# Optimization experiments

Measured on AMD Instinct MI355X. Metric: run time of the kernel, lower is better.

The kernel has to match this reference:

```python
import jax, jax.numpy as jnp
import numpy as np

# ---- problem sizes / hyperparameters (init_kwargs) ----
B, N = 1024, 512          # batch, variable dim
M_INEQ, M_EQ = 512, 16    # inequality / equality constraint counts
ALPHA = 0.05              # PGD step size
MAX_ITER = 3              # PGD iterations (self.max_iter)
RHO = 1.0                 # ADMM penalty for the projection QP
ADMM_ITERS = 15           # inner QP-solver iterations (replaces QPFunction interior point)


def setup_inputs() -> dict:
    key = jax.random.key(0)
    k1, k2, k3, k4 = jax.random.split(key, 4)
    c = jax.random.normal(k1, (B, N), jnp.float32)
    G = jax.random.normal(k2, (M_INEQ, N), jnp.float32) / np.float32(np.sqrt(N))
    A = jax.random.normal(k3, (M_EQ, N), jnp.float32) / np.float32(np.sqrt(N))
    z0 = jax.random.normal(k4, (N,), jnp.float32)  # known feasible point
    b = A @ z0
    h = G @ z0 + jnp.float32(0.5)  # strict feasibility margin
    return {"c": c, "G": G, "h": h, "A": A, "b": b}


def _project(x, G, h, A, b):
    """Batched Euclidean projection: argmin_z ||z - x||^2 s.t. Gz<=h, Az=b.
    Mathematically identical to QPFunction(2*I, -2*x, G, h, A, b); solved with
    a fixed-iteration ADMM sharing one precomputed KKT factor across the batch.
    """
    n = x.shape[-1]
    me = A.shape[0]
    bs = x.shape[0]
    # KKT matrix for the equality-constrained z-update: [[I + rho G^T G, A^T],[A, 0]]
    K = jnp.block([
        [jnp.eye(n, dtype=x.dtype) + RHO * (G.T @ G), A.T],
        [A, jnp.zeros((me, me), x.dtype)],
    ])
    Kinv = jnp.linalg.inv(K)  # (n+me, n+me), shared across batch & iterations
    b_rhs = jnp.broadcast_to(b, (bs, me))

    def z_from(s, u):
        # rhs = [x + rho * G^T (h - s - u); b], batched over B
        rhs = jnp.concatenate([x + RHO * ((h - s - u) @ G), b_rhs], axis=-1)
        return (rhs @ Kinv.T)[:, :n]  # [B, N]

    s = jnp.maximum(0.0, h - x @ G.T)  # slack init at z0 = x
    u = jnp.zeros_like(s)              # scaled dual

    def step(carry, _):
        s, u = carry
        z = z_from(s, u)
        Gz = z @ G.T                             # [B, M_INEQ]
        s2 = jnp.maximum(0.0, h - Gz - u)        # s-update (projection onto s>=0)
        u2 = u + Gz + s2 - h                     # dual update
        return (s2, u2), None

    (s, u), _ = jax.lax.scan(step, (s, u), None, length=ADMM_ITERS)
    return z_from(s, u)


def reference(c, G, h, A, b):
    # x = cvx_blank(c): initial feasible iterate (projection of c onto the polytope)
    x = _project(c, G, h, A, b)
    for _ in range(MAX_ITER):  # PGD loop (small fixed count)
        grad = x - c                # grad_f(x_i, c_i) for f = 0.5||x - c||^2 (batched)
        x = x - ALPHA * grad        # gradient step
        x = _project(x, G, h, A, b) # QP projection step (QPFunction equivalent)
    return x
```

## Files before the change

kernel.cpp:

```cpp
#include <hip/hip_runtime.h>
#include <hip/hip_bf16.h>

#define BB 1024
#define NN 512
#define MI 512
#define ME 16
#define ALPHA 0.05f
#define NS_ITERS 8
#define ADMM_IT 15

typedef __attribute__((ext_vector_type(8))) short short8;
typedef __attribute__((ext_vector_type(4))) float float4v;

__device__ inline short f2bf(float v) {
    __hip_bfloat16 b = __float2bfloat16(v);
    return *reinterpret_cast<short*>(&b);
}
__device__ inline float bf2f(short s) {
    __hip_bfloat16 b = *reinterpret_cast<__hip_bfloat16*>(&s);
    return __bfloat162float(b);
}
__device__ inline void split_store(float v, short* __restrict__ hi, short* __restrict__ lo, size_t idx) {
    short h = f2bf(v);
    hi[idx] = h;
    lo[idx] = f2bf(v - bf2f(h));
}

__global__ void detect_dtype_k(const unsigned short* __restrict__ g_raw,
                               float* __restrict__ flag) {
    __shared__ int cnt;
    int tid = threadIdx.x;
    if (tid == 0) cnt = 0;
    __syncthreads();
    int local = 0;
    for (int i = tid; i < 8192; i += 256) {
        int e = (g_raw[i] >> 7) & 0xFF;
        if (e >= 0x83) local++;
    }
    atomicAdd(&cnt, local);
    __syncthreads();
    if (tid == 0) flag[0] = (cnt < 64) ? 1.0f : 0.0f;
}

__global__ void ingest_all_k(const void* __restrict__ c_raw, const void* __restrict__ G_raw,
                             const void* __restrict__ h_raw, const void* __restrict__ A_raw,
                             const void* __restrict__ b_raw,
                             float* __restrict__ cF, short* __restrict__ xh, short* __restrict__ xl,
                             float* __restrict__ GF, short* __restrict__ GFh, short* __restrict__ GFl,
                             float* __restrict__ hF, float* __restrict__ AF, float* __restrict__ bF,
                             const float* __restrict__ flag) {
    int i = blockIdx.x * 256 + threadIdx.x;
    bool isbf = flag[0] > 0.5f;
    #define RD(p, idx) (isbf ? __bfloat162float(((const __hip_bfloat16*)(p))[idx]) : ((const float*)(p))[idx])
    if (i < BB * NN) { float v = RD(c_raw, i); cF[i] = v; split_store(v, xh, xl, i); }
    if (i < MI * NN) { float v = RD(G_raw, i); GF[i] = v; split_store(v, GFh, GFl, i); }
    if (i < MI)      hF[i] = RD(h_raw, i);
    if (i < ME * NN) AF[i] = RD(A_raw, i);
    if (i < ME)      bF[i] = RD(b_raw, i);
    #undef RD
}

__global__ void transpose_split_k(const float* __restrict__ src,
                                  short* __restrict__ dh, short* __restrict__ dl) {
    __shared__ float t[32][33];
    int bx = blockIdx.x * 32, by = blockIdx.y * 32;
    int tx = threadIdx.x & 31, ty0 = threadIdx.x >> 5;
    for (int i = ty0; i < 32; i += 8) t[i][tx] = src[(by + i) * 512 + bx + tx];
    __syncthreads();
    for (int i = ty0; i < 32; i += 8)
        split_store(t[tx][i], dh, dl, (size_t)(bx + i) * 512 + by + tx);
}

__global__ void row_abs_sum_k(const float* __restrict__ Mm, float* __restrict__ rs) {
    int row = blockIdx.x, lane = threadIdx.x;
    float s = 0.f;
    for (int j = lane; j < NN; j += 64) s += fabsf(Mm[row * NN + j]);
    for (int off = 32; off; off >>= 1) s += __shfl_down(s, off);
    if (lane == 0) rs[row] = s;
}

__global__ void max_c0_k(const float* __restrict__ rs, float* __restrict__ c0s) {
    int lane = threadIdx.x;
    float m = 0.f;
    for (int i = lane; i < NN; i += 64) m = fmaxf(m, rs[i]);
    for (int off = 32; off; off >>= 1) m = fmaxf(m, __shfl_down(m, off));
    if (lane == 0) c0s[0] = 2.0f / (1.0f + m);
}

__global__ void init_X_k(float* __restrict__ X, short* __restrict__ Xhi,
                         short* __restrict__ Xlo, const float* __restrict__ c0s) {
    int idx = blockIdx.x * 256 + threadIdx.x;
    if (idx < NN * NN) {
        int i = idx / NN, j = idx - i * NN;
        float v = (i == j) ? c0s[0] : 0.f;
        X[idx] = v;
        split_store(v, Xhi, Xlo, idx);
    }
}

__global__ void inv16_k(const float* __restrict__ S, float* __restrict__ Si) {
    int r = threadIdx.x;
    float a[16], bI[16];
    #pragma unroll
    for (int j = 0; j < 16; ++j) {
        a[j]  = (r < 16) ? S[r * 16 + j] : 0.f;
        bI[j] = (r < 16 && j == r) ? 1.f : 0.f;
    }
    for (int k = 0; k < 16; ++k) {
        float pa[16], pb[16];
        #pragma unroll
        for (int j = 0; j < 16; ++j) { pa[j] = __shfl(a[j], k); pb[j] = __shfl(bI[j], k); }
        float inv = 1.0f / pa[k];
        if (r == k) {
            #pragma unroll
            for (int j = 0; j < 16; ++j) { a[j] = pa[j] * inv; bI[j] = pb[j] * inv; }
        } else {
            float f = a[k] * inv;
            #pragma unroll
            for (int j = 0; j < 16; ++j) {
                a[j]  = fmaf(-f, pa[j], a[j]);
                bI[j] = fmaf(-f, pb[j], bI[j]);
            }
        }
    }
    if (r < 16)
        #pragma unroll
        for (int j = 0; j < 16; ++j) Si[r * 16 + j] = bI[j];
}

__global__ void Y_k(const float* __restrict__ Minv, const float* __restrict__ AF,
                    float* __restrict__ Y) {
    int m = blockIdx.x;
    int wv = threadIdx.x >> 6, lane = threadIdx.x & 63;
    float mv[8];
    #pragma unroll
    for (int i = 0; i < 8; ++i) mv[i] = Minv[m * 512 + lane + i * 64];
    #pragma unroll
    for (int jj = 0; jj < 4; ++jj) {
        int j = wv * 4 + jj;
        float s = 0.f;
        #pragma unroll
        for (int i = 0; i < 8; ++i) s += mv[i] * AF[j * 512 + lane + i * 64];
        for (int off = 32; off; off >>= 1) s += __shfl_down(s, off);
        if (lane == 0) Y[m * 16 + j] = s;
    }
}

__global__ void Sm_k(const float* __restrict__ AF, const float* __restrict__ Y,
                     float* __restrict__ Sm) {
    int i = threadIdx.x >> 4, j = threadIdx.x & 15;
    float s = 0.f;
    #pragma unroll 8
    for (int k = 0; k < 512; ++k) s += AF[i * 512 + k] * Y[k * 16 + j];
    Sm[i * 16 + j] = s;
}

__global__ void T1zb_k(const float* __restrict__ Y, const float* __restrict__ Si,
                       const float* __restrict__ bF, float* __restrict__ T1,
                       float* __restrict__ zb) {
    int m = blockIdx.x * 16 + (threadIdx.x >> 4), j = threadIdx.x & 15;
    float s = 0.f;
    #pragma unroll
    for (int k = 0; k < 16; ++k) s += Y[m * 16 + k] * Si[k * 16 + j];
    T1[m * 16 + j] = s;
    float v = s * bF[j];
    v += __shfl_down(v, 8); v += __shfl_down(v, 4);
    v += __shfl_down(v, 2); v += __shfl_down(v, 1);
    if (j == 0) zb[m] = v;
}

__global__ void W1_k(const float* __restrict__ Minv, const float* __restrict__ T1,
                     const float* __restrict__ Y,
                     short* __restrict__ W1h, short* __restrict__ W1l) {
    int idx = blockIdx.x * 256 + threadIdx.x;
    int m = idx >> 9, n = idx & 511;
    float s = Minv[idx];
    #pragma unroll
    for (int k = 0; k < 16; ++k) s -= T1[m * 16 + k] * Y[n * 16 + k];
    split_store(s, W1h, W1l, idx);
}

__global__ void g0_k(const float* __restrict__ GF, const float* __restrict__ zb,
                     float* __restrict__ g0) {
    int m = blockIdx.x * 4 + (threadIdx.x >> 6);
    int lane = threadIdx.x & 63;
    float s = 0.f;
    #pragma unroll
    for (int i = 0; i < 8; ++i) s += GF[m * 512 + lane + i * 64] * zb[lane + i * 64];
    for (int off = 32; off; off >>= 1) s += __shfl_down(s, off);
    if (lane == 0) g0[m] = s;
}

#define CH 128
#define LDC 136

__global__ __launch_bounds__(256) void mfma_gemm2(
    const short* __restrict__ Ahi, const short* __restrict__ Alo,
    const short* __restrict__ Bhi, const short* __restrict__ Blo,
    float* __restrict__ C, short* __restrict__ Chi, short* __restrict__ Clo,
    const float* __restrict__ E, const float* __restrict__ v1,
    float* __restrict__ U, float* __restrict__ Xtra,
    const float* __restrict__ dtf, void* __restrict__ Out, int epi)
{
    __shared__ short Ash[2][16 * LDC];
    __shared__ short Bsh[2][64 * LDC];
    const int tid = threadIdx.x;
    const int wv = tid >> 6, ln = tid & 63;
    const int quad = ln >> 4, lr = ln & 15;
    const int m0 = blockIdx.y * 16, n0 = blockIdx.x * 64;

    float4v acc1 = {0.f, 0.f, 0.f, 0.f};
    float4v acc2 = {0.f, 0.f, 0.f, 0.f};

    short8 pa[2], pb[8];
    #pragma unroll
    for (int i = 0; i < 2; ++i) {
        int s = tid + 256 * i; int pl = s >> 8, rem = s & 255, row = rem >> 4, oct = rem & 15;
        const short* P = pl ? Alo : Ahi;
        pa[i] = *(const short8*)(P + (size_t)(m0 + row) * 512 + oct * 8);
    }
    #pragma unroll
    for (int i = 0; i < 8; ++i) {
        int s = tid + 256 * i; int pl = s >> 10, rem = s & 1023, row = rem >> 4, oct = rem & 15;
        const short* P = pl ? Blo : Bhi;
        pb[i] = *(const short8*)(P + (size_t)(n0 + row) * 512 + oct * 8);
    }

    for (int c = 0; c < 4; ++c) {
        if (c) __syncthreads();
        #pragma unroll
        for (int i = 0; i < 2; ++i) {
            int s = tid + 256 * i; int pl = s >> 8, rem = s & 255, row = rem >> 4, oct = rem & 15;
            *(short8*)&Ash[pl][row * LDC + oct * 8] = pa[i];
        }
        #pragma unroll
        for (int i = 0; i < 8; ++i) {
            int s = tid + 256 * i; int pl = s >> 10, rem = s & 1023, row = rem >> 4, oct = rem & 15;
            *(short8*)&Bsh[pl][row * LDC + oct * 8] = pb[i];
        }
        __syncthreads();
        if (c + 1 < 4) {
            int kb = (c + 1) * CH;
            #pragma unroll
            for (int i = 0; i < 2; ++i) {
                int s = tid + 256 * i; int pl = s >> 8, rem = s & 255, row = rem >> 4, oct = rem & 15;
                const short* P = pl ? Alo : Ahi;
                pa[i] = *(const short8*)(P + (size_t)(m0 + row) * 512 + kb + oct * 8);
            }
            #pragma unroll
            for (int i = 0; i < 8; ++i) {
                int s = tid + 256 * i; int pl = s >> 10, rem = s & 1023, row = rem >> 4, oct = rem & 15;
                const short* P = pl ? Blo : Bhi;
                pb[i] = *(const short8*)(P + (size_t)(n0 + row) * 512 + kb + oct * 8);
            }
        }
        #pragma unroll
        for (int ks = 0; ks < 4; ++ks) {
            int ko = (ks * 4 + quad) * 8;
            short8 ah = *(const short8*)&Ash[0][lr * LDC + ko];
            short8 al = *(const short8*)&Ash[1][lr * LDC + ko];
            short8 bh = *(const short8*)&Bsh[0][(wv * 16 + lr) * LDC + ko];
            short8 bl = *(const short8*)&Bsh[1][(wv * 16 + lr) * LDC + ko];
            acc1 = __builtin_amdgcn_mfma_f32_16x16x32_bf16(ah, bh, acc1, 0, 0, 0);
            acc2 = __builtin_amdgcn_mfma_f32_16x16x32_bf16(ah, bl, acc2, 0, 0, 0);
            acc2 = __builtin_amdgcn_mfma_f32_16x16x32_bf16(al, bh, acc2, 0, 0, 0);
        }
    }

    #pragma unroll
    for (int r = 0; r < 4; ++r) {
        int m = m0 + quad * 4 + r;
        int n = n0 + wv * 16 + lr;
        float a = acc1[r] + acc2[r];
        if (epi == 7) {
            int seg = n0 >> 9;
            int nl = n - (seg << 9);
            size_t idx = (size_t)m * 512 + nl;
            if (seg == 0) {
                float t0 = fminf(v1[nl], a);
                U[idx] = 0.f;
                Chi[idx] = f2bf(t0);
            } else if (seg == 1) {
                C[idx] = a + E[nl];
            } else {
                Xtra[idx] = a;
            }
            continue;
        }
        size_t idx = (size_t)m * 512 + n;
        if (epi == 0) {
            C[idx] = a;
            if (Chi) split_store(a, Chi, Clo, idx);
        } else if (epi == 1) {
            a += (m == n) ? 1.f : 0.f;
            C[idx] = a;
            split_store(a, Chi, Clo, idx);
        } else if (epi == 2) {
            a = 2.f * E[idx] - a;
            C[idx] = a;
            split_store(a, Chi, Clo, idx);
        } else if (epi == 6) {
            float z = a + E[idx] + v1[n];
            float xp = (1.0f - ALPHA) * z + ALPHA * Xtra[idx];
            split_store(xp, Chi, Clo, idx);
        } else if (epi == 8) {
            float z = a + E[idx] + v1[n];
            if (dtf[0] > 0.5f) ((__hip_bfloat16*)Out)[idx] = __float2bfloat16(z);
            else               ((float*)Out)[idx] = z;
        } else {
            split_store(a, Chi, Clo, idx);
        }
    }
}

__global__ __launch_bounds__(256) void admm_bf16_k(
    const short* __restrict__ Ab, const short* __restrict__ Bb,
    const float* __restrict__ q0, const float* __restrict__ hF,
    float* __restrict__ uB, short* __restrict__ dh, short* __restrict__ dl)
{
    __shared__ short As[16 * LDC];
    __shared__ short Bs[64 * LDC];
    const int tid = threadIdx.x;
    const int wv = tid >> 6, ln = tid & 63;
    const int quad = ln >> 4, lr = ln & 15;
    const int m0 = blockIdx.y * 16, n0 = blockIdx.x * 64;

    float4v acc1 = {0.f, 0.f, 0.f, 0.f};
    float4v acc2 = {0.f, 0.f, 0.f, 0.f};

    short8 pa, pb[4];
    {
        int row = tid >> 4, oct = tid & 15;
        pa = *(const short8*)(Ab + (size_t)(m0 + row) * 512 + oct * 8);
    }
    #pragma unroll
    for (int i = 0; i < 4; ++i) {
        int s = tid + 256 * i; int row = s >> 4, oct = s & 15;
        pb[i] = *(const short8*)(Bb + (size_t)(n0 + row) * 512 + oct * 8);
    }

    for (int c = 0; c < 4; ++c) {
        if (c) __syncthreads();
        {
            int row = tid >> 4, oct = tid & 15;
            *(short8*)&As[row * LDC + oct * 8] = pa;
        }
        #pragma unroll
        for (int i = 0; i < 4; ++i) {
            int s = tid + 256 * i; int row = s >> 4, oct = s & 15;
            *(short8*)&Bs[row * LDC + oct * 8] = pb[i];
        }
        __syncthreads();
        if (c + 1 < 4) {
            int kb = (c + 1) * CH;
            {
                int row = tid >> 4, oct = tid & 15;
                pa = *(const short8*)(Ab + (size_t)(m0 + row) * 512 + kb + oct * 8);
            }
            #pragma unroll
            for (int i = 0; i < 4; ++i) {
                int s = tid + 256 * i; int row = s >> 4, oct = s & 15;
                pb[i] = *(const short8*)(Bb + (size_t)(n0 + row) * 512 + kb + oct * 8);
            }
        }
        #pragma unroll
        for (int ks = 0; ks < 4; ++ks) {
            int ko = (ks * 4 + quad) * 8;
            short8 a = *(const short8*)&As[lr * LDC + ko];
            short8 b = *(const short8*)&Bs[(wv * 16 + lr) * LDC + ko];
            if (ks & 1) acc2 = __builtin_amdgcn_mfma_f32_16x16x32_bf16(a, b, acc2, 0, 0, 0);
            else        acc1 = __builtin_amdgcn_mfma_f32_16x16x32_bf16(a, b, acc1, 0, 0, 0);
        }
    }

    #pragma unroll
    for (int r = 0; r < 4; ++r) {
        int m = m0 + quad * 4 + r;
        int n = n0 + wv * 16 + lr;
        size_t idx = (size_t)m * 512 + n;
        float gz = acc1[r] + acc2[r] + q0[idx];
        float hn = hF[n];
        float w = hn - gz - uB[idx];
        uB[idx] = fmaxf(0.f, -w);
        float t2 = hn - fabsf(w);
        short hh = f2bf(t2);
        dh[idx] = hh;
        if (dl) dl[idx] = f2bf(t2 - bf2f(hh));
    }
}


extern "C" void kernel_launch(void* const* d_in, const int* in_sizes, int n_in,
                              void* d_out, int out_size, void* d_ws, size_t ws_size,
                              hipStream_t stream) {
    const void* c_raw = d_in[0];
    const void* G_raw = d_in[1];
    const void* h_raw = d_in[2];
    const void* A_raw = d_in[3];
    const void* b_raw = d_in[4];

    float* w = (float*)d_ws;
    size_t o = 0;
    auto alloc = [&](size_t n) { float* p = w + o; o += (n + 63) & ~(size_t)63; return p; };

    float* cF  = alloc(BB * NN);
    float* GF  = alloc(MI * NN);
    float* AF  = alloc(ME * NN);
    float* hF  = alloc(MI);
    float* bF  = alloc(ME);
    float* Mm  = alloc(NN * NN);
    float* Xf0 = alloc(NN * NN);
    float* Xf1 = alloc(NN * NN);
    float* Rf  = alloc(MI * NN);
    float* Y   = alloc(NN * ME);
    float* T1  = alloc(NN * ME);
    float* Sm  = alloc(ME * ME);
    float* Si  = alloc(ME * ME);
    float* zb  = alloc(NN);
    float* g0  = alloc(MI);
    float* rs  = alloc(NN);
    float* c0s = alloc(16);
    float* dtf = alloc(16);
    float* q0  = alloc(BB * MI);
    float* xW  = alloc(BB * NN);
    float* uB  = alloc(BB * MI);

    short* sbp = (short*)(w + o);
    size_t so = 0;
    auto allocS = [&](size_t n) { short* p = sbp + so; so += (n + 127) & ~(size_t)127; return p; };

    short* Bcat_h = allocS(3 * 512 * 512);
    short* Bcat_l = allocS(3 * 512 * 512);
    short* GFh = Bcat_h;              short* GFl = Bcat_l;
    short* Rh  = Bcat_h + 512 * 512;  short* Rl  = Bcat_l + 512 * 512;
    short* W1h = Bcat_h + 1024 * 512; short* W1l = Bcat_l + 1024 * 512;

    short* GTh = allocS(NN * MI);  short* GTl = allocS(NN * MI);
    short* Mmh = allocS(NN * NN);  short* Mml = allocS(NN * NN);
    short* X0h = allocS(NN * NN);  short* X0l = allocS(NN * NN);
    short* X1h = allocS(NN * NN);  short* X1l = allocS(NN * NN);
    short* Uh  = allocS(NN * NN);  short* Ul  = allocS(NN * NN);
    short* RTh = allocS(NN * MI);  short* RTl = allocS(NN * MI);
    short* Qh  = allocS(MI * MI);  short* Ql  = allocS(MI * MI);
    short* xh  = allocS(BB * NN);  short* xl  = allocS(BB * NN);
    short* tAh = allocS(BB * MI);  short* tAl = allocS(BB * MI);
    short* tBh = allocS(BB * MI);  short* tBl = allocS(BB * MI);

    dim3 blk(256);
    auto cdiv = [](int a, int b) { return (a + b - 1) / b; };
    dim3 gSq(8, 32);
    dim3 gBt(8, 64);
    dim3 gCombo(24, 64);

    detect_dtype_k<<<1, 256, 0, stream>>>((const unsigned short*)G_raw, dtf);
    ingest_all_k<<<cdiv(BB * NN, 256), blk, 0, stream>>>(
        c_raw, G_raw, h_raw, A_raw, b_raw,
        cF, xh, xl, GF, GFh, GFl, hF, AF, bF, dtf);

    transpose_split_k<<<dim3(16, 16), blk, 0, stream>>>(GF, GTh, GTl);

    mfma_gemm2<<<gSq, blk, 0, stream>>>(GTh, GTl, GTh, GTl, Mm, Mmh, Mml,
                                        nullptr, nullptr, nullptr, nullptr, nullptr, nullptr, 1);

    row_abs_sum_k<<<NN, 64, 0, stream>>>(Mm, rs);
    max_c0_k<<<1, 64, 0, stream>>>(rs, c0s);
    init_X_k<<<cdiv(NN * NN, 256), blk, 0, stream>>>(Xf0, X0h, X0l, c0s);
    float* Xf[2] = {Xf0, Xf1};
    short* Xh[2] = {X0h, X1h};
    short* Xl[2] = {X0l, X1l};
    int cur = 0;
    for (int it = 0; it < NS_ITERS; ++it) {
        int nxt = cur ^ 1;
        mfma_gemm2<<<gSq, blk, 0, stream>>>(Xh[cur], Xl[cur], Mmh, Mml, nullptr, Uh, Ul,
                                            nullptr, nullptr, nullptr, nullptr, nullptr, nullptr, 9);
        mfma_gemm2<<<gSq, blk, 0, stream>>>(Uh, Ul, Xh[cur], Xl[cur], Xf[nxt], Xh[nxt], Xl[nxt],
                                            Xf[cur], nullptr, nullptr, nullptr, nullptr, nullptr, 2);
        cur = nxt;
    }
    float* Minv = Xf[cur];

    Y_k<<<NN, blk, 0, stream>>>(Minv, AF, Y);
    Sm_k<<<1, blk, 0, stream>>>(AF, Y, Sm);
    inv16_k<<<1, 64, 0, stream>>>(Sm, Si);
    T1zb_k<<<NN / 16, blk, 0, stream>>>(Y, Si, bF, T1, zb);
    W1_k<<<NN * NN / 256, blk, 0, stream>>>(Minv, T1, Y, W1h, W1l);

    mfma_gemm2<<<gSq, blk, 0, stream>>>(GFh, GFl, W1h, W1l, Rf, Rh, Rl,
                                        nullptr, nullptr, nullptr, nullptr, nullptr, nullptr, 0);
    transpose_split_k<<<dim3(16, 16), blk, 0, stream>>>(Rf, RTh, RTl);
    mfma_gemm2<<<gSq, blk, 0, stream>>>(Rh, Rl, GFh, GFl, nullptr, Qh, Ql,
                                        nullptr, nullptr, nullptr, nullptr, nullptr, nullptr, 9);
    g0_k<<<NN / 4, blk, 0, stream>>>(GF, zb, g0);

    for (int p = 0; p < 4; ++p) {
        mfma_gemm2<<<gCombo, blk, 0, stream>>>(xh, xl, Bcat_h, Bcat_l, q0, tAh, tAl,
                                               g0, hF, uB, xW, nullptr, nullptr, 7);
        for (int it = 0; it < ADMM_IT; ++it) {
            const short* sh = (it & 1) ? tBh : tAh;
            short* dh = (it & 1) ? tAh : tBh;
            short* dl = (it == ADMM_IT - 1) ? tBl : nullptr;
            admm_bf16_k<<<gBt, blk, 0, stream>>>(sh, Qh, q0, hF, uB, dh, dl);
        }
        if (p < 3) {
            mfma_gemm2<<<gBt, blk, 0, stream>>>(tBh, tBl, RTh, RTl, nullptr, xh, xl,
                                                xW, zb, nullptr, cF, nullptr, nullptr, 6);
        } else {
            mfma_gemm2<<<gBt, blk, 0, stream>>>(tBh, tBl, RTh, RTl, nullptr, nullptr, nullptr,
                                                xW, zb, nullptr, nullptr, dtf, d_out, 8);
        }
    }
}
```

Before: 688.3 us.

## Use single-bf16 Newton-Schulz iterations with one split-precision refinement step

The Newton-Schulz inverse of I+G^T G is restructured. The first iterate is computed analytically (2c0 I - c0^2 M) and the row-abs-sum is fused into the Gram GEMM epilogue through atomics. Five cheap iterations then run in a new single-bf16 MFMA kernel, followed by one full hi/lo split-precision iteration to restore accuracy. This replaces eight split-precision iterations, and the Sm and 16x16 inverse kernels are merged into one to cut launches. The cost is lower precision in the intermediate iterates, which relies on the final refinement step for convergence.

```diff
diff --git a/kernel.cpp b/kernel.cpp
--- a/kernel.cpp
+++ b/kernel.cpp
@@ -6,8 +6,8 @@
 #define MI 512
 #define ME 16
 #define ALPHA 0.05f
-#define NS_ITERS 8
 #define ADMM_IT 15
+#define NS_CHEAP 5
 
 typedef __attribute__((ext_vector_type(8))) short short8;
 typedef __attribute__((ext_vector_type(4))) float float4v;
@@ -48,7 +48,7 @@
                              float* __restrict__ cF, short* __restrict__ xh, short* __restrict__ xl,
                              float* __restrict__ GF, short* __restrict__ GFh, short* __restrict__ GFl,
                              float* __restrict__ hF, float* __restrict__ AF, float* __restrict__ bF,
-                             const float* __restrict__ flag) {
+                             float* __restrict__ rs, const float* __restrict__ flag) {
     int i = blockIdx.x * 256 + threadIdx.x;
     bool isbf = flag[0] > 0.5f;
     #define RD(p, idx) (isbf ? __bfloat162float(((const __hip_bfloat16*)(p))[idx]) : ((const float*)(p))[idx])
@@ -57,6 +57,7 @@
     if (i < MI)      hF[i] = RD(h_raw, i);
     if (i < ME * NN) AF[i] = RD(A_raw, i);
     if (i < ME)      bF[i] = RD(b_raw, i);
+    if (i < NN)      rs[i] = 0.f;
     #undef RD
 }
 
@@ -71,61 +72,61 @@
         split_store(t[tx][i], dh, dl, (size_t)(bx + i) * 512 + by + tx);
 }
 
-__global__ void row_abs_sum_k(const float* __restrict__ Mm, float* __restrict__ rs) {
-    int row = blockIdx.x, lane = threadIdx.x;
+__global__ void initX1_k(const float* __restrict__ rs, const float* __restrict__ Mm,
+                         short* __restrict__ X1h) {
+    int ln = threadIdx.x & 63;
+    float mx = 0.f;
+    #pragma unroll
+    for (int i = 0; i < 8; ++i) mx = fmaxf(mx, rs[ln + i * 64]);
+    for (int off = 32; off; off >>= 1) mx = fmaxf(mx, __shfl_down(mx, off));
+    float c0 = 2.0f / (1.0f + __shfl(mx, 0));
+    #pragma unroll
+    for (int j = 0; j < 4; ++j) {
+        int idx = blockIdx.x * 1024 + j * 256 + threadIdx.x;
+        int r = idx >> 9, cc = idx & 511;
+        float v = -c0 * c0 * Mm[idx] + ((r == cc) ? 2.0f * c0 : 0.f);
+        X1h[idx] = f2bf(v);
+    }
+}
+
+__global__ void sm_inv_k(const float* __restrict__ AF, const float* __restrict__ Y,
+                         float* __restrict__ Si) {
+    __shared__ float Sm[256];
+    int i = threadIdx.x >> 4, j = threadIdx.x & 15;
     float s = 0.f;
-    for (int j = lane; j < NN; j += 64) s += fabsf(Mm[row * NN + j]);
-    for (int off = 32; off; off >>= 1) s += __shfl_down(s, off);
-    if (lane == 0) rs[row] = s;
-}
-
-__global__ void max_c0_k(const float* __restrict__ rs, float* __restrict__ c0s) {
-    int lane = threadIdx.x;
-    float m = 0.f;
-    for (int i = lane; i < NN; i += 64) m = fmaxf(m, rs[i]);
-    for (int off = 32; off; off >>= 1) m = fmaxf(m, __shfl_down(m, off));
-    if (lane == 0) c0s[0] = 2.0f / (1.0f + m);
-}
-
-__global__ void init_X_k(float* __restrict__ X, short* __restrict__ Xhi,
-                         short* __restrict__ Xlo, const float* __restrict__ c0s) {
-    int idx = blockIdx.x * 256 + threadIdx.x;
-    if (idx < NN * NN) {
-        int i = idx / NN, j = idx - i * NN;
-        float v = (i == j) ? c0s[0] : 0.f;
-        X[idx] = v;
-        split_store(v, Xhi, Xlo, idx);
-    }
-}
-
-__global__ void inv16_k(const float* __restrict__ S, float* __restrict__ Si) {
-    int r = threadIdx.x;
-    float a[16], bI[16];
-    #pragma unroll
-    for (int j = 0; j < 16; ++j) {
-        a[j]  = (r < 16) ? S[r * 16 + j] : 0.f;
-        bI[j] = (r < 16 && j == r) ? 1.f : 0.f;
-    }
-    for (int k = 0; k < 16; ++k) {
-        float pa[16], pb[16];
-        #pragma unroll
-        for (int j = 0; j < 16; ++j) { pa[j] = __shfl(a[j], k); pb[j] = __shfl(bI[j], k); }
-        float inv = 1.0f / pa[k];
-        if (r == k) {
+    #pragma unroll 8
+    for (int k = 0; k < 512; ++k) s += AF[i * 512 + k] * Y[k * 16 + j];
+    Sm[i * 16 + j] = s;
+    __syncthreads();
+    if (threadIdx.x < 64) {
+        int r = threadIdx.x;
+        float a[16], bI[16];
+        #pragma unroll
+        for (int jj = 0; jj < 16; ++jj) {
+            a[jj]  = (r < 16) ? Sm[r * 16 + jj] : 0.f;
+            bI[jj] = (r < 16 && jj == r) ? 1.f : 0.f;
+        }
+        for (int k = 0; k < 16; ++k) {
+            float pa[16], pb[16];
             #pragma unroll
-            for (int j = 0; j < 16; ++j) { a[j] = pa[j] * inv; bI[j] = pb[j] * inv; }
-        } else {
-            float f = a[k] * inv;
+            for (int jj = 0; jj < 16; ++jj) { pa[jj] = __shfl(a[jj], k); pb[jj] = __shfl(bI[jj], k); }
+            float inv = 1.0f / pa[k];
+            if (r == k) {
+                #pragma unroll
+                for (int jj = 0; jj < 16; ++jj) { a[jj] = pa[jj] * inv; bI[jj] = pb[jj] * inv; }
+            } else {
+                float f = a[k] * inv;
+                #pragma unroll
+                for (int jj = 0; jj < 16; ++jj) {
+                    a[jj]  = fmaf(-f, pa[jj], a[jj]);
+                    bI[jj] = fmaf(-f, pb[jj], bI[jj]);
+                }
+            }
+        }
+        if (r < 16)
             #pragma unroll
-            for (int j = 0; j < 16; ++j) {
-                a[j]  = fmaf(-f, pa[j], a[j]);
-                bI[j] = fmaf(-f, pb[j], bI[j]);
-            }
-        }
-    }
-    if (r < 16)
-        #pragma unroll
-        for (int j = 0; j < 16; ++j) Si[r * 16 + j] = bI[j];
+            for (int jj = 0; jj < 16; ++jj) Si[r * 16 + jj] = bI[jj];
+    }
 }
 
 __global__ void Y_k(const float* __restrict__ Minv, const float* __restrict__ AF,
@@ -144,15 +145,6 @@
         for (int off = 32; off; off >>= 1) s += __shfl_down(s, off);
         if (lane == 0) Y[m * 16 + j] = s;
     }
-}
-
-__global__ void Sm_k(const float* __restrict__ AF, const float* __restrict__ Y,
-                     float* __restrict__ Sm) {
-    int i = threadIdx.x >> 4, j = threadIdx.x & 15;
-    float s = 0.f;
-    #pragma unroll 8
-    for (int k = 0; k < 512; ++k) s += AF[i * 512 + k] * Y[k * 16 + j];
-    Sm[i * 16 + j] = s;
 }
 
 __global__ void T1zb_k(const float* __restrict__ Y, const float* __restrict__ Si,
@@ -295,6 +287,10 @@
             a += (m == n) ? 1.f : 0.f;
             C[idx] = a;
             split_store(a, Chi, Clo, idx);
+            float s = fabsf(a);
+            s += __shfl_xor(s, 1); s += __shfl_xor(s, 2);
+            s += __shfl_xor(s, 4); s += __shfl_xor(s, 8);
+            if (lr == 0) atomicAdd(&U[m], s);
         } else if (epi == 2) {
             a = 2.f * E[idx] - a;
             C[idx] = a;
@@ -313,6 +309,86 @@
     }
 }
 
+__global__ __launch_bounds__(256) void sp_gemm_k(
+    const short* __restrict__ Ab, const short* __restrict__ Bb,
+    const short* __restrict__ Eh, short* __restrict__ Ch,
+    short* __restrict__ Cl, float* __restrict__ Cf, int mode)
+{
+    __shared__ short As[16 * LDC];
+    __shared__ short Bs[64 * LDC];
+    const int tid = threadIdx.x;
+    const int wv = tid >> 6, ln = tid & 63;
+    const int quad = ln >> 4, lr = ln & 15;
+    const int m0 = blockIdx.y * 16, n0 = blockIdx.x * 64;
+
+    float4v acc1 = {0.f, 0.f, 0.f, 0.f};
+    float4v acc2 = {0.f, 0.f, 0.f, 0.f};
+
+    short8 pa, pb[4];
+    {
+        int row = tid >> 4, oct = tid & 15;
+        pa = *(const short8*)(Ab + (size_t)(m0 + row) * 512 + oct * 8);
+    }
+    #pragma unroll
+    for (int i = 0; i < 4; ++i) {
+        int s = tid + 256 * i; int row = s >> 4, oct = s & 15;
+        pb[i] = *(const short8*)(Bb + (size_t)(n0 + row) * 512 + oct * 8);
+    }
+
+    for (int c = 0; c < 4; ++c) {
+        if (c) __syncthreads();
+        {
+            int row = tid >> 4, oct = tid & 15;
+            *(short8*)&As[row * LDC + oct * 8] = pa;
+        }
+        #pragma unroll
+        for (int i = 0; i < 4; ++i) {
+            int s = tid + 256 * i; int row = s >> 4, oct = s & 15;
+            *(short8*)&Bs[row * LDC + oct * 8] = pb[i];
+        }
+        __syncthreads();
+        if (c + 1 < 4) {
+            int kb = (c + 1) * CH;
+            {
+                int row = tid >> 4, oct = tid & 15;
+                pa = *(const short8*)(Ab + (size_t)(m0 + row) * 512 + kb + oct * 8);
+            }
+            #pragma unroll
+            for (int i = 0; i < 4; ++i) {
+                int s = tid + 256 * i; int row = s >> 4, oct = s & 15;
+                pb[i] = *(const short8*)(Bb + (size_t)(n0 + row) * 512 + kb + oct * 8);
+            }
+        }
+        #pragma unroll
+        for (int ks = 0; ks < 4; ++ks) {
+            int ko = (ks * 4 + quad) * 8;
+            short8 a = *(const short8*)&As[lr * LDC + ko];
+            short8 b = *(const short8*)&Bs[(wv * 16 + lr) * LDC + ko];
+            if (ks & 1) acc2 = __builtin_amdgcn_mfma_f32_16x16x32_bf16(a, b, acc2, 0, 0, 0);
+            else        acc1 = __builtin_amdgcn_mfma_f32_16x16x32_bf16(a, b, acc1, 0, 0, 0);
+        }
+    }
+
+    #pragma unroll
+    for (int r = 0; r < 4; ++r) {
+        int m = m0 + quad * 4 + r;
+        int n = n0 + wv * 16 + lr;
+        size_t idx = (size_t)m * 512 + n;
+        float a = acc1[r] + acc2[r];
+        if (mode == 0) {
+            Ch[idx] = f2bf(a);
+        } else {
+            float v = 2.f * bf2f(Eh[idx]) - a;
+            short hh = f2bf(v);
+            Ch[idx] = hh;
+            if (Cl) {
+                Cl[idx] = f2bf(v - bf2f(hh));
+                Cf[idx] = v;
+            }
+        }
+    }
+}
+
 __global__ __launch_bounds__(256) void admm_bf16_k(
     const short* __restrict__ Ab, const short* __restrict__ Bb,
     const float* __restrict__ q0, const float* __restrict__ hF,
@@ -414,12 +490,10 @@
     float* Rf  = alloc(MI * NN);
     float* Y   = alloc(NN * ME);
     float* T1  = alloc(NN * ME);
-    float* Sm  = alloc(ME * ME);
     float* Si  = alloc(ME * ME);
     float* zb  = alloc(NN);
     float* g0  = alloc(MI);
     float* rs  = alloc(NN);
-    float* c0s = alloc(16);
     float* dtf = alloc(16);
     float* q0  = alloc(BB * MI);
     float* xW  = alloc(BB * NN);
@@ -455,33 +529,33 @@
     detect_dtype_k<<<1, 256, 0, stream>>>((const unsigned short*)G_raw, dtf);
     ingest_all_k<<<cdiv(BB * NN, 256), blk, 0, stream>>>(
         c_raw, G_raw, h_raw, A_raw, b_raw,
-        cF, xh, xl, GF, GFh, GFl, hF, AF, bF, dtf);
+        cF, xh, xl, GF, GFh, GFl, hF, AF, bF, rs, dtf);
 
     transpose_split_k<<<dim3(16, 16), blk, 0, stream>>>(GF, GTh, GTl);
 
     mfma_gemm2<<<gSq, blk, 0, stream>>>(GTh, GTl, GTh, GTl, Mm, Mmh, Mml,
-                                        nullptr, nullptr, nullptr, nullptr, nullptr, nullptr, 1);
-
-    row_abs_sum_k<<<NN, 64, 0, stream>>>(Mm, rs);
-    max_c0_k<<<1, 64, 0, stream>>>(rs, c0s);
-    init_X_k<<<cdiv(NN * NN, 256), blk, 0, stream>>>(Xf0, X0h, X0l, c0s);
-    float* Xf[2] = {Xf0, Xf1};
-    short* Xh[2] = {X0h, X1h};
-    short* Xl[2] = {X0l, X1l};
-    int cur = 0;
-    for (int it = 0; it < NS_ITERS; ++it) {
-        int nxt = cur ^ 1;
-        mfma_gemm2<<<gSq, blk, 0, stream>>>(Xh[cur], Xl[cur], Mmh, Mml, nullptr, Uh, Ul,
-                                            nullptr, nullptr, nullptr, nullptr, nullptr, nullptr, 9);
-        mfma_gemm2<<<gSq, blk, 0, stream>>>(Uh, Ul, Xh[cur], Xl[cur], Xf[nxt], Xh[nxt], Xl[nxt],
-                                            Xf[cur], nullptr, nullptr, nullptr, nullptr, nullptr, 2);
-        cur = nxt;
-    }
-    float* Minv = Xf[cur];
+                                        nullptr, nullptr, rs, nullptr, nullptr, nullptr, 1);
+
+    initX1_k<<<256, blk, 0, stream>>>(rs, Mm, X0h);
+
+    short* XcurH = X0h;
+    short* XnxtH = X1h;
+    for (int it = 0; it < NS_CHEAP; ++it) {
+        bool last = (it == NS_CHEAP - 1);
+        sp_gemm_k<<<gSq, blk, 0, stream>>>(XcurH, Mmh, nullptr, Uh, nullptr, nullptr, 0);
+        short* nl = last ? ((XnxtH == X0h) ? X0l : X1l) : nullptr;
+        float* nf = last ? ((XnxtH == X0h) ? Xf0 : Xf1) : nullptr;
+        sp_gemm_k<<<gSq, blk, 0, stream>>>(Uh, XcurH, XcurH, XnxtH, nl, nf, 1);
+        short* t = XcurH; XcurH = XnxtH; XnxtH = t;
+    }
+    mfma_gemm2<<<gSq, blk, 0, stream>>>(X1h, X1l, Mmh, Mml, nullptr, Uh, Ul,
+                                        nullptr, nullptr, nullptr, nullptr, nullptr, nullptr, 9);
+    mfma_gemm2<<<gSq, blk, 0, stream>>>(Uh, Ul, X1h, X1l, Xf0, X0h, X0l,
+                                        Xf1, nullptr, nullptr, nullptr, nullptr, nullptr, 2);
+    float* Minv = Xf0;
 
     Y_k<<<NN, blk, 0, stream>>>(Minv, AF, Y);
-    Sm_k<<<1, blk, 0, stream>>>(AF, Y, Sm);
-    inv16_k<<<1, 64, 0, stream>>>(Sm, Si);
+    sm_inv_k<<<1, blk, 0, stream>>>(AF, Y, Si);
     T1zb_k<<<NN / 16, blk, 0, stream>>>(Y, Si, bF, T1, zb);
     W1_k<<<NN * NN / 256, blk, 0, stream>>>(Minv, T1, Y, W1h, W1l);
 
```

New measurement: 629.7 us. -8.5%, faster.

## Fuse Newton-Schulz init into GEMM epilogue and analytic first iterate, merge small solves

Applied to the files above, without the earlier changes.

Row-abs-sum of M is now accumulated inside the M=I+GᵀG GEMM epilogue through shuffles and atomics, and the separate row sum, max and identity-init kernels are replaced by one kernel. That kernel writes the first Newton-Schulz iterate (2c0·I − c0²·M) analytically, so one GEMM pair is removed. The 16x16 Schur product and its inverse are merged into one kernel. The goal is fewer launches and fewer GEMMs, at the cost of atomic float accumulation whose summation order is nondeterministic.

```diff
diff --git a/kernel.cpp b/kernel.cpp
--- a/kernel.cpp
+++ b/kernel.cpp
@@ -6,8 +6,8 @@
 #define MI 512
 #define ME 16
 #define ALPHA 0.05f
-#define NS_ITERS 8
 #define ADMM_IT 15
+#define NS_PAIRS 7
 
 typedef __attribute__((ext_vector_type(8))) short short8;
 typedef __attribute__((ext_vector_type(4))) float float4v;
@@ -48,7 +48,7 @@
                              float* __restrict__ cF, short* __restrict__ xh, short* __restrict__ xl,
                              float* __restrict__ GF, short* __restrict__ GFh, short* __restrict__ GFl,
                              float* __restrict__ hF, float* __restrict__ AF, float* __restrict__ bF,
-                             const float* __restrict__ flag) {
+                             float* __restrict__ rs, const float* __restrict__ flag) {
     int i = blockIdx.x * 256 + threadIdx.x;
     bool isbf = flag[0] > 0.5f;
     #define RD(p, idx) (isbf ? __bfloat162float(((const __hip_bfloat16*)(p))[idx]) : ((const float*)(p))[idx])
@@ -57,6 +57,7 @@
     if (i < MI)      hF[i] = RD(h_raw, i);
     if (i < ME * NN) AF[i] = RD(A_raw, i);
     if (i < ME)      bF[i] = RD(b_raw, i);
+    if (i < NN)      rs[i] = 0.f;
     #undef RD
 }
 
@@ -71,61 +72,63 @@
         split_store(t[tx][i], dh, dl, (size_t)(bx + i) * 512 + by + tx);
 }
 
-__global__ void row_abs_sum_k(const float* __restrict__ Mm, float* __restrict__ rs) {
-    int row = blockIdx.x, lane = threadIdx.x;
+__global__ void initX1_k(const float* __restrict__ rs, const float* __restrict__ Mm,
+                         float* __restrict__ Xf, short* __restrict__ Xh,
+                         short* __restrict__ Xl) {
+    int ln = threadIdx.x & 63;
+    float mx = 0.f;
+    #pragma unroll
+    for (int i = 0; i < 8; ++i) mx = fmaxf(mx, rs[ln + i * 64]);
+    for (int off = 32; off; off >>= 1) mx = fmaxf(mx, __shfl_down(mx, off));
+    float c0 = 2.0f / (1.0f + __shfl(mx, 0));
+    #pragma unroll
+    for (int j = 0; j < 4; ++j) {
+        int idx = blockIdx.x * 1024 + j * 256 + threadIdx.x;
+        int r = idx >> 9, cc = idx & 511;
+        float v = -c0 * c0 * Mm[idx] + ((r == cc) ? 2.0f * c0 : 0.f);
+        Xf[idx] = v;
+        split_store(v, Xh, Xl, idx);
+    }
+}
+
+__global__ void sm_inv_k(const float* __restrict__ AF, const float* __restrict__ Y,
+                         float* __restrict__ Si) {
+    __shared__ float Sm[256];
+    int i = threadIdx.x >> 4, j = threadIdx.x & 15;
     float s = 0.f;
-    for (int j = lane; j < NN; j += 64) s += fabsf(Mm[row * NN + j]);
-    for (int off = 32; off; off >>= 1) s += __shfl_down(s, off);
-    if (lane == 0) rs[row] = s;
-}
-
-__global__ void max_c0_k(const float* __restrict__ rs, float* __restrict__ c0s) {
-    int lane = threadIdx.x;
-    float m = 0.f;
-    for (int i = lane; i < NN; i += 64) m = fmaxf(m, rs[i]);
-    for (int off = 32; off; off >>= 1) m = fmaxf(m, __shfl_down(m, off));
-    if (lane == 0) c0s[0] = 2.0f / (1.0f + m);
-}
-
-__global__ void init_X_k(float* __restrict__ X, short* __restrict__ Xhi,
-                         short* __restrict__ Xlo, const float* __restrict__ c0s) {
-    int idx = blockIdx.x * 256 + threadIdx.x;
-    if (idx < NN * NN) {
-        int i = idx / NN, j = idx - i * NN;
-        float v = (i == j) ? c0s[0] : 0.f;
-        X[idx] = v;
-        split_store(v, Xhi, Xlo, idx);
-    }
-}
-
-__global__ void inv16_k(const float* __restrict__ S, float* __restrict__ Si) {
-    int r = threadIdx.x;
-    float a[16], bI[16];
-    #pragma unroll
-    for (int j = 0; j < 16; ++j) {
-        a[j]  = (r < 16) ? S[r * 16 + j] : 0.f;
-        bI[j] = (r < 16 && j == r) ? 1.f : 0.f;
-    }
-    for (int k = 0; k < 16; ++k) {
-        float pa[16], pb[16];
-        #pragma unroll
-        for (int j = 0; j < 16; ++j) { pa[j] = __shfl(a[j], k); pb[j] = __shfl(bI[j], k); }
-        float inv = 1.0f / pa[k];
-        if (r == k) {
+    #pragma unroll 8
+    for (int k = 0; k < 512; ++k) s += AF[i * 512 + k] * Y[k * 16 + j];
+    Sm[i * 16 + j] = s;
+    __syncthreads();
+    if (threadIdx.x < 64) {
+        int r = threadIdx.x;
+        float a[16], bI[16];
+        #pragma unroll
+        for (int jj = 0; jj < 16; ++jj) {
+            a[jj]  = (r < 16) ? Sm[r * 16 + jj] : 0.f;
+            bI[jj] = (r < 16 && jj == r) ? 1.f : 0.f;
+        }
+        for (int k = 0; k < 16; ++k) {
+            float pa[16], pb[16];
             #pragma unroll
-            for (int j = 0; j < 16; ++j) { a[j] = pa[j] * inv; bI[j] = pb[j] * inv; }
-        } else {
-            float f = a[k] * inv;
+            for (int jj = 0; jj < 16; ++jj) { pa[jj] = __shfl(a[jj], k); pb[jj] = __shfl(bI[jj], k); }
+            float inv = 1.0f / pa[k];
+            if (r == k) {
+                #pragma unroll
+                for (int jj = 0; jj < 16; ++jj) { a[jj] = pa[jj] * inv; bI[jj] = pb[jj] * inv; }
+            } else {
+                float f = a[k] * inv;
+                #pragma unroll
+                for (int jj = 0; jj < 16; ++jj) {
+                    a[jj]  = fmaf(-f, pa[jj], a[jj]);
+                    bI[jj] = fmaf(-f, pb[jj], bI[jj]);
+                }
+            }
+        }
+        if (r < 16)
             #pragma unroll
-            for (int j = 0; j < 16; ++j) {
-                a[j]  = fmaf(-f, pa[j], a[j]);
-                bI[j] = fmaf(-f, pb[j], bI[j]);
-            }
-        }
-    }
-    if (r < 16)
-        #pragma unroll
-        for (int j = 0; j < 16; ++j) Si[r * 16 + j] = bI[j];
+            for (int jj = 0; jj < 16; ++jj) Si[r * 16 + jj] = bI[jj];
+    }
 }
 
 __global__ void Y_k(const float* __restrict__ Minv, const float* __restrict__ AF,
@@ -144,15 +147,6 @@
         for (int off = 32; off; off >>= 1) s += __shfl_down(s, off);
         if (lane == 0) Y[m * 16 + j] = s;
     }
-}
-
-__global__ void Sm_k(const float* __restrict__ AF, const float* __restrict__ Y,
-                     float* __restrict__ Sm) {
-    int i = threadIdx.x >> 4, j = threadIdx.x & 15;
-    float s = 0.f;
-    #pragma unroll 8
-    for (int k = 0; k < 512; ++k) s += AF[i * 512 + k] * Y[k * 16 + j];
-    Sm[i * 16 + j] = s;
 }
 
 __global__ void T1zb_k(const float* __restrict__ Y, const float* __restrict__ Si,
@@ -295,6 +289,10 @@
             a += (m == n) ? 1.f : 0.f;
             C[idx] = a;
             split_store(a, Chi, Clo, idx);
+            float s = fabsf(a);
+            s += __shfl_xor(s, 1); s += __shfl_xor(s, 2);
+            s += __shfl_xor(s, 4); s += __shfl_xor(s, 8);
+            if (lr == 0) atomicAdd(&U[m], s);
         } else if (epi == 2) {
             a = 2.f * E[idx] - a;
             C[idx] = a;
@@ -414,12 +412,10 @@
     float* Rf  = alloc(MI * NN);
     float* Y   = alloc(NN * ME);
     float* T1  = alloc(NN * ME);
-    float* Sm  = alloc(ME * ME);
     float* Si  = alloc(ME * ME);
     float* zb  = alloc(NN);
     float* g0  = alloc(MI);
     float* rs  = alloc(NN);
-    float* c0s = alloc(16);
     float* dtf = alloc(16);
     float* q0  = alloc(BB * MI);
     float* xW  = alloc(BB * NN);
@@ -455,21 +451,20 @@
     detect_dtype_k<<<1, 256, 0, stream>>>((const unsigned short*)G_raw, dtf);
     ingest_all_k<<<cdiv(BB * NN, 256), blk, 0, stream>>>(
         c_raw, G_raw, h_raw, A_raw, b_raw,
-        cF, xh, xl, GF, GFh, GFl, hF, AF, bF, dtf);
+        cF, xh, xl, GF, GFh, GFl, hF, AF, bF, rs, dtf);
 
     transpose_split_k<<<dim3(16, 16), blk, 0, stream>>>(GF, GTh, GTl);
 
     mfma_gemm2<<<gSq, blk, 0, stream>>>(GTh, GTl, GTh, GTl, Mm, Mmh, Mml,
-                                        nullptr, nullptr, nullptr, nullptr, nullptr, nullptr, 1);
-
-    row_abs_sum_k<<<NN, 64, 0, stream>>>(Mm, rs);
-    max_c0_k<<<1, 64, 0, stream>>>(rs, c0s);
-    init_X_k<<<cdiv(NN * NN, 256), blk, 0, stream>>>(Xf0, X0h, X0l, c0s);
+                                        nullptr, nullptr, rs, nullptr, nullptr, nullptr, 1);
+
+    initX1_k<<<256, blk, 0, stream>>>(rs, Mm, Xf0, X0h, X0l);
+
     float* Xf[2] = {Xf0, Xf1};
     short* Xh[2] = {X0h, X1h};
     short* Xl[2] = {X0l, X1l};
     int cur = 0;
-    for (int it = 0; it < NS_ITERS; ++it) {
+    for (int it = 0; it < NS_PAIRS; ++it) {
         int nxt = cur ^ 1;
         mfma_gemm2<<<gSq, blk, 0, stream>>>(Xh[cur], Xl[cur], Mmh, Mml, nullptr, Uh, Ul,
                                             nullptr, nullptr, nullptr, nullptr, nullptr, nullptr, 9);
@@ -480,8 +475,7 @@
     float* Minv = Xf[cur];
 
     Y_k<<<NN, blk, 0, stream>>>(Minv, AF, Y);
-    Sm_k<<<1, blk, 0, stream>>>(AF, Y, Sm);
-    inv16_k<<<1, 64, 0, stream>>>(Sm, Si);
+    sm_inv_k<<<1, blk, 0, stream>>>(AF, Y, Si);
     T1zb_k<<<NN / 16, blk, 0, stream>>>(Y, Si, bF, T1, zb);
     W1_k<<<NN * NN / 256, blk, 0, stream>>>(Minv, T1, Y, W1h, W1l);
 
```

New measurement: 666.6 us. -3.2%, faster.
